# Optimization experiments

Hardware: AMD Instinct MI355X
Metric: run time of the kernel (lower is better)

## Reference

```python
import jax, jax.numpy as jnp
import numpy as np
from jax import lax

N, K, T_OBS, PRED = 64, 48, 30, 15
EMB, NODE, EDGE, ATT, CNN = 64, 128, 256, 64, 512


def setup_inputs():
    key = jax.random.key(0)
    ks = jax.random.split(key, 18)
    rn = lambda k, s, sc=1.0: jax.random.normal(k, s, jnp.float32) * sc
    return {
        "img_embedding": rn(ks[0], (N, CNN)),
        "target_obs_pos_abs": rn(ks[1], (N, T_OBS, 2)),
        "target_obs_pos_rel": rn(ks[2], (N, T_OBS, 2)),
        "target_obs_pos_step": rn(ks[3], (N, T_OBS, 2), 0.1),
        "nearby_obs_pos_abs": rn(ks[4], (N, K, T_OBS, 2)),
        "nearby_obs_pos_rel": rn(ks[5], (N, K, T_OBS, 2)),
        "nearby_obs_pos_step": rn(ks[6], (N, K, T_OBS, 2), 0.1),
        "target_obs_hist_size": jax.random.randint(ks[7], (N, 1), 0, T_OBS),
        "nearby_obs_hist_sizes": jax.random.randint(ks[8], (N, K, 1), 0, T_OBS),
        "W_disp": rn(ks[9], (EMB, 2), 0.1), "b_disp": jnp.zeros((EMB,), jnp.float32),
        "Wih_t": rn(ks[10], (4 * NODE, EMB), 0.05), "Whh_t": rn(ks[11], (4 * NODE, NODE), 0.05),
        "bih_t": jnp.zeros((4 * NODE,), jnp.float32), "bhh_t": jnp.zeros((4 * NODE,), jnp.float32),
        "Wih_n": rn(ks[12], (4 * EDGE, EMB), 0.05), "Whh_n": rn(ks[13], (4 * EDGE, EDGE), 0.05),
        "bih_n": jnp.zeros((4 * EDGE,), jnp.float32), "bhh_n": jnp.zeros((4 * EDGE,), jnp.float32),
        "W_att_t": rn(ks[14], (ATT, 2), 0.1), "b_att_t": jnp.zeros((ATT,), jnp.float32),
        "W_att_n": rn(ks[15], (ATT, 2), 0.1), "b_att_n": jnp.zeros((ATT,), jnp.float32),
        "W_pred": rn(ks[16], (2, NODE + CNN + EDGE), 0.02), "b_pred": jnp.zeros((2,), jnp.float32),
    }


def _lstm_cell(x, h, c, Wih, Whh, bih, bhh):
    # PyTorch LSTM gate order: i, f, g, o
    g = x @ Wih.T + h @ Whh.T + bih + bhh
    i, f, gg, o = jnp.split(g, 4, axis=-1)
    c2 = jax.nn.sigmoid(f) * c + jax.nn.sigmoid(i) * jnp.tanh(gg)
    return jax.nn.sigmoid(o) * jnp.tanh(c2), c2


def _forward(img_embedding, target_obs_pos_abs, target_obs_pos_rel, target_obs_pos_step,
             nearby_obs_pos_abs, nearby_obs_pos_rel, nearby_obs_pos_step,
             W_disp, b_disp, Wih_t, Whh_t, bih_t, bhh_t, Wih_n, Whh_n, bih_n, bhh_n,
             W_att_t, b_att_t, W_att_n, b_att_n, W_pred, b_pred,
             target_obs_hist_size, nearby_obs_hist_sizes):
    t_hist = target_obs_hist_size[:, 0]          # [N]
    n_hist = nearby_obs_hist_sizes[:, :, 0]      # [N, K]
    M = N * K

    def step(carry, t):
        tht, tct, nht, nct, Ht, cabs, crel, cstep, nabs, nstep = carry
        is_obs = t < T_OBS
        tc = jnp.minimum(t, T_OBS - 1)
        # prediction branch (only takes effect when t >= T_OBS)
        pred_out = jnp.concatenate([tht, img_embedding, Ht], 1) @ W_pred.T + b_pred  # [N,2]
        cabs = jnp.where(is_obs, target_obs_pos_abs[:, tc], cabs + pred_out)
        crel = jnp.where(is_obs, target_obs_pos_rel[:, tc], crel + pred_out)
        cstep = jnp.where(is_obs, target_obs_pos_step[:, tc], pred_out)
        nabs = jnp.where(is_obs, nearby_obs_pos_abs[:, :, tc], nabs)
        nstep = jnp.where(is_obs, nearby_obs_pos_step[:, :, tc], nstep)
        tmask = jnp.where(is_obs, t_hist > T_OBS - t, True)   # [N] bool
        nmask = jnp.where(is_obs, n_hist > T_OBS - t, True)   # [N,K] bool
        gate_t = jnp.sum(tmask) > 0  # emulates 'continue' when no target observed
        # target LSTM step, masked scatter-back
        th2, tc2 = _lstm_cell(cstep @ W_disp.T + b_disp, tht, tct, Wih_t, Whh_t, bih_t, bhh_t)
        u = (tmask & gate_t)[:, None]
        tht = jnp.where(u, th2, tht)
        tct = jnp.where(u, tc2, tct)
        # nearby LSTM step, masked scatter-back
        currN = jnp.sum(nmask)
        gate_n = gate_t & (currN > 0)
        nh2, nc2 = _lstm_cell(nstep.reshape(M, 2) @ W_disp.T + b_disp, nht, nct, Wih_n, Whh_n, bih_n, bhh_n)
        un = (nmask.reshape(M) & gate_n)[:, None]
        nht = jnp.where(un, nh2, nht)
        nct = jnp.where(un, nc2, nct)
        # social attention over padded nearby dim
        an = (nabs - cabs[:, None, :]) @ W_att_n.T + b_att_n   # [N,K,ATT]
        at = crel @ W_att_t.T + b_att_t                        # [N,ATT]
        mf = nmask.astype(jnp.float32)
        sc = jnp.einsum('nka,na->nk', an, at) * currN.astype(jnp.float32) / jnp.sqrt(jnp.float32(ATT))
        sc = sc * mf
        num = jnp.exp(sc - jnp.max(sc, 1, keepdims=True)) * mf
        w = num / (jnp.sum(num, 1, keepdims=True) + 1e-6)
        Ht = jnp.where(gate_n, jnp.einsum('nke,nk->ne', nht.reshape(N, K, EDGE), w), Ht)
        return (tht, tct, nht, nct, Ht, cabs, crel, cstep, nabs, nstep), crel

    z = lambda s: jnp.zeros(s, jnp.float32)
    init = (z((N, NODE)), z((N, NODE)), z((M, EDGE)), z((M, EDGE)), z((N, EDGE)),
            z((N, 2)), z((N, 2)), z((N, 2)), z((N, K, 2)), z((N, K, 2)))
    _, rels = lax.scan(step, init, jnp.arange(1, T_OBS + PRED))
    # last PRED emitted crel values are pred_traj[:, 0:PRED]
    return jnp.transpose(rels[-PRED:], (1, 0, 2))


def reference(img_embedding, target_obs_pos_abs, target_obs_pos_rel, target_obs_pos_step,
              nearby_obs_pos_abs, nearby_obs_pos_rel, nearby_obs_pos_step,
              target_obs_hist_size, nearby_obs_hist_sizes,
              W_disp, b_disp, Wih_t, Whh_t, bih_t, bhh_t, Wih_n, Whh_n, bih_n, bhh_n,
              W_att_t, b_att_t, W_att_n, b_att_n, W_pred, b_pred):
    return _forward(img_embedding, target_obs_pos_abs, target_obs_pos_rel, target_obs_pos_step,
                    nearby_obs_pos_abs, nearby_obs_pos_rel, nearby_obs_pos_step,
                    W_disp, b_disp, Wih_t, Whh_t, bih_t, bhh_t, Wih_n, Whh_n, bih_n, bhh_n,
                    W_att_t, b_att_t, W_att_n, b_att_n, W_pred, b_pred,
                    target_obs_hist_size, nearby_obs_hist_sizes)
```

## Files before the change

kernel.cpp:

```cpp
#include <hip/hip_runtime.h>
#include <math.h>

#define NT 64
#define KN 48
#define TOBS 30
#define NPRED 15
#define EMB 64
#define NODE 128
#define EDGE 256
#define ATTD 64
#define CNN 512
#define GNN 1024
#define GTT 512
#define TMAX 44

typedef _Float16 f16;
typedef f16 f16x8 __attribute__((ext_vector_type(8)));
typedef f16 f16x2 __attribute__((ext_vector_type(2)));
typedef float f32x4 __attribute__((ext_vector_type(4)));

__device__ __forceinline__ float rcp_f(float x) { return __builtin_amdgcn_rcpf(x); }
__device__ __forceinline__ float sigm(float x) { return rcp_f(1.f + __expf(-x)); }
__device__ __forceinline__ float tanh_f(float x) {
  float xx = fminf(fmaxf(x, -20.f), 20.f);
  float e = __expf(-2.f * xx);
  return (1.f - e) * rcp_f(1.f + e);
}
__device__ __forceinline__ unsigned ldcoh(const unsigned* p) {
  return __hip_atomic_load(p, __ATOMIC_RELAXED, __HIP_MEMORY_SCOPE_AGENT);
}
__device__ __forceinline__ float ldcohf(const float* p) {
  unsigned u = __hip_atomic_load((const unsigned*)p, __ATOMIC_RELAXED, __HIP_MEMORY_SCOPE_AGENT);
  return __builtin_bit_cast(float, u);
}
__device__ __forceinline__ void stcoh(unsigned* p, unsigned v) {
  __hip_atomic_store(p, v, __ATOMIC_RELAXED, __HIP_MEMORY_SCOPE_AGENT);
}
__device__ __forceinline__ void stcohf(float* p, float v) {
  __hip_atomic_store((unsigned*)p, __builtin_bit_cast(unsigned, v),
                     __ATOMIC_RELAXED, __HIP_MEMORY_SCOPE_AGENT);
}

__global__ __launch_bounds__(512) void prep_kernel(
    const float* __restrict__ Wih_n, const float* __restrict__ Whh_n,
    const float* __restrict__ bih_n, const float* __restrict__ bhh_n,
    const float* __restrict__ Wih_t, const float* __restrict__ Whh_t,
    const float* __restrict__ bih_t, const float* __restrict__ bhh_t,
    const float* __restrict__ W_disp, const float* __restrict__ b_disp,
    const int* __restrict__ t_hist, const int* __restrict__ n_hist,
    f16* __restrict__ Wn, f16* __restrict__ Wt, float* __restrict__ Ptv,
    float* __restrict__ bias_n, float* __restrict__ bias_t,
    int* __restrict__ gt_arr, int* __restrict__ gn_arr, float* __restrict__ cn_arr,
    int* __restrict__ last29p, unsigned* __restrict__ flags)
{
  const int gid = blockIdx.x * 512 + threadIdx.x;
  const int nthr = gridDim.x * 512;
  __shared__ int sgn[TMAX + 1];

  if (gid < 2 * NT) flags[gid] = 0u;

  for (int idx = gid; idx < GNN * 288; idx += nthr) {
    const int j    = idx & 7;
    const int lane = (idx >> 3) & 63;
    const int g    = (idx >> 9) & 3;
    const int r    = idx >> 11;
    const int u    = r % 9;
    const int s    = r / 9;
    const int w    = s & 7;
    const int h    = s >> 3;
    const int col = g * 256 + h * 128 + w * 16 + (lane & 15);
    float v = 0.f;
    if (u == 0) {
      if ((lane >> 4) == 0 && j < 3) {
        float acc = 0.f;
        for (int e = 0; e < EMB; ++e) {
          const float sel = (j == 0) ? W_disp[e * 2]
                          : (j == 1) ? W_disp[e * 2 + 1] : b_disp[e];
          acc += sel * Wih_n[col * EMB + e];
        }
        v = acc;
      }
    } else {
      const int k = (u - 1) * 32 + (lane >> 4) * 8 + j;
      v = Whh_n[col * EDGE + k];
    }
    Wn[idx] = (f16)v;
  }
  for (int idx = gid; idx < GTT * 192; idx += nthr) {
    const int j = idx & 7;
    const int col = (idx >> 3) & 511;
    const int c8 = idx >> 12;
    const int k = c8 * 8 + j;
    const float v = (k < EMB) ? Wih_t[col * EMB + k] : Whh_t[col * NODE + (k - EMB)];
    Wt[idx] = (f16)v;
  }
  for (int idx = gid; idx < 3 * GTT; idx += nthr) {
    const int sel = idx / GTT;
    const int col = idx - sel * GTT;
    float acc = 0.f;
    for (int e = 0; e < EMB; ++e) {
      const float sv = (sel == 0) ? W_disp[e * 2]
                     : (sel == 1) ? W_disp[e * 2 + 1] : b_disp[e];
      acc += sv * Wih_t[col * EMB + e];
    }
    Ptv[sel * GTT + col] = acc;
  }
  for (int idx = gid; idx < GNN; idx += nthr) bias_n[idx] = bih_n[idx] + bhh_n[idx];
  for (int idx = gid; idx < GTT; idx += nthr) bias_t[idx] = bih_t[idx] + bhh_t[idx];

  if (blockIdx.x == 0 && threadIdx.x < 352) {
    const int t = (threadIdx.x >> 3) + 1;
    const int part = threadIdx.x & 7;
    int any_t = 0, cnt = 0;
    if (t < TOBS) {
      const int thr = TOBS - t;
      for (int nn = part; nn < NT; nn += 8) any_t |= (t_hist[nn] > thr) ? 1 : 0;
      for (int m = part; m < NT * KN; m += 8) cnt += (n_hist[m] > thr) ? 1 : 0;
    } else { any_t = (part == 0); cnt = (part == 0) ? NT * KN : 0; }
    #pragma unroll
    for (int off = 1; off < 8; off <<= 1) {
      any_t |= __shfl_xor(any_t, off);
      cnt   += __shfl_xor(cnt, off);
    }
    if (part == 0) {
      const int gn = (any_t && cnt > 0) ? 1 : 0;
      gt_arr[t] = any_t;
      gn_arr[t] = gn;
      cn_arr[t] = (float)cnt;
      sgn[t] = gn;
    }
  }
  __syncthreads();
  if (blockIdx.x == 0 && threadIdx.x == 0) {
    int l = 30;
    for (int t = 29; t >= 1; --t) if (sgn[t]) { l = t; break; }
    last29p[0] = l;
  }
}

__global__ __launch_bounds__(512, 2) void model_kernel(
    const float* __restrict__ img, const float* __restrict__ tabs,
    const float* __restrict__ trel, const float* __restrict__ tstep,
    const float* __restrict__ nabs_g, const float* __restrict__ nstep_g,
    const int* __restrict__ thist_g, const int* __restrict__ nhist_g,
    const float* __restrict__ W_att_t, const float* __restrict__ b_att_t,
    const float* __restrict__ W_att_n, const float* __restrict__ b_att_n,
    const float* __restrict__ W_pred, const float* __restrict__ b_pred,
    const f16* __restrict__ Wn, const f16* __restrict__ Wt,
    const float* __restrict__ Ptv,
    const float* __restrict__ bias_n, const float* __restrict__ bias_t,
    const int* __restrict__ gt_arr, const int* __restrict__ gn_arr,
    const float* __restrict__ cn_arr, const int* __restrict__ last29p,
    unsigned* __restrict__ flags, unsigned* __restrict__ Hglob,
    float* __restrict__ Tglob,
    float* __restrict__ out)
{
  __shared__ f16 s_wlds[3 * 16384];
  __shared__ f16 s_virt[KN][32];
  __shared__ f16 Ah[KN][264];
  __shared__ float s_tht[NODE];
  __shared__ float s_tct[64];
  __shared__ f16  s_th16[NODE];
  __shared__ float s_Ht[EDGE];
  __shared__ float s_g[256];
  __shared__ float s_bt[256];
  __shared__ float s_sc[KN], s_w[KN];
  __shared__ float s_scal[8];
  __shared__ float s_dd[4];
  __shared__ float s_pimg[2];
  __shared__ int   s_nh[KN];
  __shared__ float s_wp[2][384];
  __shared__ float s_wan0[ATTD], s_wan1[ATTD], s_ban[ATTD];
  __shared__ float s_wat0[ATTD], s_wat1[ATTD], s_bat[ATTD];

  const int tid  = threadIdx.x;
  const int n    = blockIdx.x & 63;
  const int hb   = blockIdx.x >> 6;
  const int w    = tid >> 6;
  const int lane = tid & 63;
  const int cl   = lane & 15;
  const int kq   = lane >> 4;
  const int koff = kq * 8;

  for (int i = tid; i < KN * 264; i += 512) ((f16*)Ah)[i] = (f16)0.f;
  for (int i = tid; i < KN * 32; i += 512)
    s_virt[i >> 5][i & 31] = ((i & 31) == 2) ? (f16)1.f : (f16)0.f;
  for (int i = tid; i < NODE; i += 512) { s_tht[i] = 0.f; s_th16[i] = (f16)0.f; }
  if (tid < 64) s_tct[tid] = 0.f;
  for (int i = tid; i < EDGE; i += 512) s_Ht[i] = 0.f;
  if (tid < 256) {
    const int g = tid >> 6, dl = tid & 63;
    s_bt[tid] = bias_t[g * 128 + hb * 64 + dl];
  }
  for (int i = tid; i < 768; i += 512) {
    const int ww = i / 384, j = i - ww * 384;
    s_wp[ww][j] = (j < 128) ? W_pred[ww * 896 + j] : W_pred[ww * 896 + 640 + (j - 128)];
  }
  if (tid < KN) s_nh[tid] = nhist_g[n * KN + tid];
  if (tid < 8) s_scal[tid] = 0.f;
  if (tid >= 64 && tid < 128) {
    const int a = tid - 64;
    s_wan0[a] = W_att_n[a * 2]; s_wan1[a] = W_att_n[a * 2 + 1]; s_ban[a] = b_att_n[a];
  }
  if (tid >= 128 && tid < 192) {
    const int a = tid - 128;
    s_wat0[a] = W_att_t[a * 2]; s_wat1[a] = W_att_t[a * 2 + 1]; s_bat[a] = b_att_t[a];
  }
  const int thist = thist_g[n];
  const int last29 = last29p[0];

  float pt0 = 0.f, pt1 = 0.f, ptb = 0.f;
  if (tid < 256) {
    const int col = (tid >> 6) * 128 + hb * 64 + (tid & 63);
    pt0 = Ptv[col]; pt1 = Ptv[512 + col]; ptb = Ptv[1024 + col];
  }

  for (int i = tid; i < 3 * 8 * 256; i += 512) {
    const int c  = i & 255;
    const int wv = (i >> 8) & 7;
    const int u  = i >> 11;
    const size_t gbase = ((size_t)((hb * 8 + wv) * 9 + u)) * 2048;
    *(f16x8*)(s_wlds + (size_t)(u * 8 + wv) * 2048 + c * 8) =
        *(const f16x8*)(Wn + gbase + c * 8);
  }

  if (w < 2) {
    float s = 0.f;
    for (int j = lane; j < CNN; j += 64) s += img[n * CNN + j] * W_pred[w * 896 + 128 + j];
    for (int off = 32; off; off >>= 1) s += __shfl_down(s, off);
    if (lane == 0) s_pimg[w] = s + b_pred[w];
  }

  float creg[3][4];
  #pragma unroll
  for (int b = 0; b < 3; ++b)
    #pragma unroll
    for (int c = 0; c < 4; ++c) creg[b][c] = 0.f;

  float bias_q[4];
  #pragma unroll
  for (int g = 0; g < 4; ++g) bias_q[g] = bias_n[g * 256 + hb * 128 + w * 16 + cl];

  const f16* gW = Wn + ((size_t)(hb * 8 + w) * 9) * 2048 + (size_t)lane * 8;
  const f16* lW = s_wlds + (size_t)w * 2048 + (size_t)lane * 8;
  const int e_g = hb * 128 + w * 16 + cl;
  unsigned* myflag = flags + n * 2 + hb;
  unsigned* otflag = flags + n * 2 + (1 - hb);
  int bn = 0;

  __syncthreads();

  {
    if (tid < 96) {
      const int row = tid >> 1, comp = tid & 1;
      s_virt[row][comp] = (f16)nstep_g[((n * KN + row) * TOBS + 1) * 2 + comp];
    }
    if (tid < 2) {
      s_scal[tid]     = tabs[(n * TOBS + 1) * 2 + tid];
      s_scal[2 + tid] = trel[(n * TOBS + 1) * 2 + tid];
      s_scal[4 + tid] = tstep[(n * TOBS + 1) * 2 + tid];
    }
    if (tid >= 384 && tid < 448) {
      const int a = tid - 384;
      const float r0 = trel[(n * TOBS + 1) * 2 + 0], r1 = trel[(n * TOBS + 1) * 2 + 1];
      const float at = r0 * s_wat0[a] + r1 * s_wat1[a] + s_bat[a];
      float p0 = at * s_wan0[a], p1 = at * s_wan1[a], pb = at * s_ban[a];
      #pragma unroll
      for (int off = 32; off; off >>= 1) {
        p0 += __shfl_xor(p0, off); p1 += __shfl_xor(p1, off); pb += __shfl_xor(pb, off);
      }
      if (a == 0) { s_dd[0] = p0; s_dd[1] = p1; s_dd[2] = pb; }
    }
  }
  __syncthreads();

  for (int t = 1; t <= TMAX; ++t) {
    const bool is_obs = (t < TOBS);
    const int tc = is_obs ? t : (TOBS - 1);
    const int gate_t = gt_arr[t];
    const int gate_n = gn_arr[t];
    const float currN = cn_arr[t];
    const bool tmask = is_obs ? (thist > (TOBS - t)) : true;
    const bool do_t = gate_t && tmask;
    const bool need_x = (gate_n || do_t);
    const bool do_att = gate_n && (t >= last29);
    const int par = bn & 1;

    if (!is_obs) {
      if (w < 2) {
        float s = 0.f;
        for (int j = lane; j < NODE; j += 64) s += s_tht[j] * s_wp[w][j];
        for (int j = lane; j < EDGE; j += 64) s += s_Ht[j] * s_wp[w][128 + j];
        for (int off = 32; off; off >>= 1) s += __shfl_down(s, off);
        if (lane == 0) {
          const float p = s + s_pimg[w];
          const float cabs = s_scal[w] + p;
          const float crel = s_scal[2 + w] + p;
          s_scal[w] = cabs; s_scal[2 + w] = crel; s_scal[4 + w] = p;
          if (hb == 0) out[(n * NPRED + (t - TOBS)) * 2 + w] = crel;
        }
      }
      __syncthreads();
      if (tid >= 384 && tid < 448) {
        const int a = tid - 384;
        const float at = s_scal[2] * s_wat0[a] + s_scal[3] * s_wat1[a] + s_bat[a];
        float p0 = at * s_wan0[a], p1 = at * s_wan1[a], pb = at * s_ban[a];
        #pragma unroll
        for (int off = 32; off; off >>= 1) {
          p0 += __shfl_xor(p0, off); p1 += __shfl_xor(p1, off); pb += __shfl_xor(pb, off);
        }
        if (a == 0) { s_dd[0] = p0; s_dd[1] = p1; s_dd[2] = pb; }
      }
      __syncthreads();
    }

    f16 hreg[3][4];
    if (gate_n) {
      f32x4 acc[3][4];
      #pragma unroll
      for (int rt = 0; rt < 3; ++rt)
        #pragma unroll
        for (int g = 0; g < 4; ++g) acc[rt][g] = (f32x4){0.f, 0.f, 0.f, 0.f};

      #pragma unroll
      for (int u = 0; u < 9; ++u) {
        f16x8 bf[4];
        if (u < 3) {
          #pragma unroll
          for (int g = 0; g < 4; ++g)
            bf[g] = *(const f16x8*)(lW + u * 16384 + g * 512);
        } else {
          #pragma unroll
          for (int g = 0; g < 4; ++g)
            bf[g] = *(const f16x8*)(gW + u * 2048 + g * 512);
        }
        f16x8 af[3];
        #pragma unroll
        for (int rt = 0; rt < 3; ++rt) {
          const int row = rt * 16 + cl;
          const f16* ap = (u == 0) ? &s_virt[row][koff]
                                   : &Ah[row][(u - 1) * 32 + koff];
          af[rt] = *(const f16x8*)ap;
        }
        #pragma unroll
        for (int g = 0; g < 4; ++g)
          #pragma unroll
          for (int rt = 0; rt < 3; ++rt)
            acc[rt][g] = __builtin_amdgcn_mfma_f32_16x16x32_f16(af[rt], bf[g], acc[rt][g], 0, 0, 0);
      }

      unsigned* Hg = Hglob + (size_t)(par * NT + n) * (KN * 128);
      #pragma unroll
      for (int rt = 0; rt < 3; ++rt) {
        #pragma unroll
        for (int jj = 0; jj < 4; ++jj) {
          const int row = rt * 16 + kq * 4 + jj;
          const bool nm = is_obs ? (s_nh[row] > (TOBS - t)) : true;
          f16 hv;
          if (nm) {
            const float iv = acc[rt][0][jj] + bias_q[0];
            const float fv = acc[rt][1][jj] + bias_q[1];
            const float gv = acc[rt][2][jj] + bias_q[2];
            const float ov = acc[rt][3][jj] + bias_q[3];
            const float c2 = sigm(fv) * creg[rt][jj] + sigm(iv) * tanh_f(gv);
            creg[rt][jj] = c2;
            hv = (f16)(sigm(ov) * tanh_f(c2));
          } else {
            hv = Ah[row][e_g];
          }
          hreg[rt][jj] = hv;
          const unsigned lo = (unsigned)__builtin_bit_cast(unsigned short, hv);
          const unsigned hi = (unsigned)__shfl_down((int)lo, 1);
          if (!(cl & 1))
            stcoh(Hg + row * 128 + (e_g >> 1), lo | (hi << 16));
        }
      }
    }

    if (do_t && tid < 256) {
      float g0 = s_bt[tid] + s_scal[4] * pt0 + s_scal[5] * pt1 + ptb;
      float g1 = 0.f, g2 = 0.f, g3 = 0.f;
      const f16x2* th2 = (const f16x2*)s_th16;
      const f16x8* wp = (const f16x8*)(Wt + ((tid >> 6) * 128 + hb * 64 + (tid & 63)) * 8);
      #pragma unroll
      for (int c8 = 0; c8 < 16; ++c8) {
        const f16x8 wv = wp[(c8 + 8) * 512];
        f16x2 w0 = {wv[0], wv[1]}, w1 = {wv[2], wv[3]};
        f16x2 w2 = {wv[4], wv[5]}, w3 = {wv[6], wv[7]};
        g0 = __builtin_amdgcn_fdot2(w0, th2[c8 * 4 + 0], g0, false);
        g1 = __builtin_amdgcn_fdot2(w1, th2[c8 * 4 + 1], g1, false);
        g2 = __builtin_amdgcn_fdot2(w2, th2[c8 * 4 + 2], g2, false);
        g3 = __builtin_amdgcn_fdot2(w3, th2[c8 * 4 + 3], g3, false);
      }
      s_g[tid] = (g0 + g1) + (g2 + g3);
    }
    if (do_att && tid >= 256 && tid < 256 + KN) {
      const int k = tid - 256;
      const float a0 = nabs_g[((n * KN + k) * TOBS + tc) * 2 + 0] - s_scal[0];
      const float a1 = nabs_g[((n * KN + k) * TOBS + tc) * 2 + 1] - s_scal[1];
      const bool nm = is_obs ? (s_nh[k] > (TOBS - t)) : true;
      const float sc = (a0 * s_dd[0] + a1 * s_dd[1] + s_dd[2]) * currN * 0.125f;
      s_sc[k] = nm ? sc : 0.f;
      s_w[k]  = nm ? 1.f : 0.f;
    }
    __syncthreads();

    if (do_t && tid < 64) {
      const int d = hb * 64 + tid;
      const float iv = s_g[tid], fv = s_g[64 + tid];
      const float gv = s_g[128 + tid], ov = s_g[192 + tid];
      const float c2 = sigm(fv) * s_tct[tid] + sigm(iv) * tanh_f(gv);
      s_tct[tid] = c2;
      const float nh = sigm(ov) * tanh_f(c2);
      s_tht[d] = nh;
      s_th16[d] = (f16)nh;
      stcohf(Tglob + ((size_t)(par * NT + n) * 2 + hb) * 64 + tid, nh);
    }
    if (do_att && w == 4) {
      const bool act = lane < KN;
      const float sc = act ? s_sc[lane] : -1.0e30f;
      const float mf = act ? s_w[lane] : 0.f;
      float mx = sc;
      #pragma unroll
      for (int off = 32; off; off >>= 1) mx = fmaxf(mx, __shfl_xor(mx, off));
      float num = __expf(sc - mx) * mf;
      float sum = num;
      #pragma unroll
      for (int off = 32; off; off >>= 1) sum += __shfl_xor(sum, off);
      if (act) s_w[lane] = num * rcp_f(sum + 1e-6f);
    }
    __syncthreads();

    if (need_x && tid == 0) {
      stcoh(myflag, (unsigned)(bn + 1));
    }

    {
      const int tn = t + 1;
      if (tn <= TOBS) {
        const int tcn = (tn < TOBS) ? tn : (TOBS - 1);
        if (tid < 96) {
          const int row = tid >> 1, comp = tid & 1;
          s_virt[row][comp] = (f16)nstep_g[((n * KN + row) * TOBS + tcn) * 2 + comp];
        }
      }
      if (tn < TOBS) {
        if (tid < 2) {
          s_scal[tid]     = tabs[(n * TOBS + tn) * 2 + tid];
          s_scal[2 + tid] = trel[(n * TOBS + tn) * 2 + tid];
          s_scal[4 + tid] = tstep[(n * TOBS + tn) * 2 + tid];
        }
        if (tid >= 384 && tid < 448) {
          const int a = tid - 384;
          const float r0 = trel[(n * TOBS + tn) * 2 + 0], r1 = trel[(n * TOBS + tn) * 2 + 1];
          const float at = r0 * s_wat0[a] + r1 * s_wat1[a] + s_bat[a];
          float p0 = at * s_wan0[a], p1 = at * s_wan1[a], pb = at * s_ban[a];
          #pragma unroll
          for (int off = 32; off; off >>= 1) {
            p0 += __shfl_xor(p0, off); p1 += __shfl_xor(p1, off); pb += __shfl_xor(pb, off);
          }
          if (a == 0) { s_dd[0] = p0; s_dd[1] = p1; s_dd[2] = pb; }
        }
      }
    }

    if (need_x && tid == 0) {
      const unsigned step = (unsigned)(bn + 1);
      while (ldcoh(otflag) < step)
        __builtin_amdgcn_s_sleep(1);
    }
    __syncthreads();

    if (gate_n) {
      const unsigned* Hg = Hglob + (size_t)(par * NT + n) * (KN * 128);
      const int ob = (1 - hb) * 64;
      for (int i = tid; i < KN * 64; i += 512) {
        const int row = i >> 6, c = i & 63;
        const unsigned v = ldcoh(Hg + row * 128 + ob + c);
        *(unsigned*)&Ah[row][(ob + c) * 2] = v;
      }
      #pragma unroll
      for (int rt = 0; rt < 3; ++rt)
        #pragma unroll
        for (int jj = 0; jj < 4; ++jj)
          Ah[rt * 16 + kq * 4 + jj][e_g] = hreg[rt][jj];
    }
    if (do_t && tid >= 448) {
      const int dl = tid - 448;
      const int d = (1 - hb) * 64 + dl;
      const float nh = ldcohf(Tglob + ((size_t)(par * NT + n) * 2 + (1 - hb)) * 64 + dl);
      s_tht[d] = nh;
      s_th16[d] = (f16)nh;
    }
    __syncthreads();

    if (do_att && tid < EDGE) {
      float h0 = 0.f, h1 = 0.f, h2 = 0.f, h3 = 0.f;
      #pragma unroll
      for (int k = 0; k < KN; k += 4) {
        h0 += (float)Ah[k][tid]     * s_w[k];
        h1 += (float)Ah[k + 1][tid] * s_w[k + 1];
        h2 += (float)Ah[k + 2][tid] * s_w[k + 2];
        h3 += (float)Ah[k + 3][tid] * s_w[k + 3];
      }
      s_Ht[tid] = (h0 + h1) + (h2 + h3);
    }
    if (need_x) bn++;
    if (t >= 29) __syncthreads();
  }
}

extern "C" void kernel_launch(void* const* d_in, const int* in_sizes, int n_in,
                              void* d_out, int out_size, void* d_ws, size_t ws_size,
                              hipStream_t stream) {
  const float* img    = (const float*)d_in[0];
  const float* tabs   = (const float*)d_in[1];
  const float* trel   = (const float*)d_in[2];
  const float* tstep  = (const float*)d_in[3];
  const float* nabs   = (const float*)d_in[4];
  const float* nstep  = (const float*)d_in[6];
  const int*   thist  = (const int*)d_in[7];
  const int*   nhist  = (const int*)d_in[8];
  const float* W_disp = (const float*)d_in[9];
  const float* b_disp = (const float*)d_in[10];
  const float* Wih_t  = (const float*)d_in[11];
  const float* Whh_t  = (const float*)d_in[12];
  const float* bih_t  = (const float*)d_in[13];
  const float* bhh_t  = (const float*)d_in[14];
  const float* Wih_n  = (const float*)d_in[15];
  const float* Whh_n  = (const float*)d_in[16];
  const float* bih_n  = (const float*)d_in[17];
  const float* bhh_n  = (const float*)d_in[18];
  const float* W_att_t = (const float*)d_in[19];
  const float* b_att_t = (const float*)d_in[20];
  const float* W_att_n = (const float*)d_in[21];
  const float* b_att_n = (const float*)d_in[22];
  const float* W_pred  = (const float*)d_in[23];
  const float* b_pred  = (const float*)d_in[24];

  char* ws = (char*)d_ws;
  f16*      Wn      = (f16*)(ws);
  f16*      Wt      = (f16*)(ws + 655360);
  float*    bias_n  = (float*)(ws + 851968);
  float*    bias_t  = (float*)(ws + 856064);
  int*      gt_arr  = (int*)(ws + 858112);
  int*      gn_arr  = (int*)(ws + 858304);
  float*    cn_arr  = (float*)(ws + 858496);
  int*      last29p = (int*)(ws + 859648);
  unsigned* flags   = (unsigned*)(ws + 860160);
  float*    Ptv     = (float*)(ws + 901120);
  unsigned* Hglob   = (unsigned*)(ws + 1048576);
  float*    Tglob   = (float*)(ws + 4194304);

  prep_kernel<<<64, 512, 0, stream>>>(Wih_n, Whh_n, bih_n, bhh_n, Wih_t, Whh_t,
                                      bih_t, bhh_t, W_disp, b_disp,
                                      thist, nhist, Wn, Wt, Ptv,
                                      bias_n, bias_t, gt_arr, gn_arr, cn_arr,
                                      last29p, flags);
  model_kernel<<<2 * NT, 512, 0, stream>>>(img, tabs, trel, tstep, nabs, nstep,
                                           thist, nhist,
                                           W_att_t, b_att_t, W_att_n, b_att_n,
                                           W_pred, b_pred,
                                           Wn, Wt, Ptv, bias_n, bias_t,
                                           gt_arr, gn_arr, cn_arr, last29p,
                                           flags, Hglob, Tglob,
                                           (float*)d_out);
}
```

Measured before the change: 634.6 us.

## Read peer half of edge hidden state directly from global in MFMA loop

Stops staging the partner block's half of the edge-LSTM hidden state into LDS each step. The MFMA A-fragments and the attention-weighted sum now load that half straight from the coherent global buffer, and only the block's own half stays in a smaller LDS array. This removes a bulk copy pass from the per-step critical section and shrinks LDS use. In exchange the inner GEMM loop issues scalar coherent global loads, which have higher latency than LDS reads, and the global H buffer is now zeroed in the prep kernel.

```diff
diff --git a/kernel.cpp b/kernel.cpp
--- a/kernel.cpp
+++ b/kernel.cpp
@@ -40,6 +40,16 @@
   __hip_atomic_store((unsigned*)p, __builtin_bit_cast(unsigned, v),
                      __ATOMIC_RELAXED, __HIP_MEMORY_SCOPE_AGENT);
 }
+__device__ __forceinline__ f16x8 ld_hpair4(const unsigned* p) {
+  union { unsigned u4[4]; f16x8 v; } cv;
+  cv.u4[0] = ldcoh(p);     cv.u4[1] = ldcoh(p + 1);
+  cv.u4[2] = ldcoh(p + 2); cv.u4[3] = ldcoh(p + 3);
+  return cv.v;
+}
+__device__ __forceinline__ float f16half(unsigned wv, int hi) {
+  unsigned short s = (unsigned short)(hi ? (wv >> 16) : (wv & 0xffffu));
+  return (float)__builtin_bit_cast(f16, s);
+}
 
 __global__ __launch_bounds__(512) void prep_kernel(
     const float* __restrict__ Wih_n, const float* __restrict__ Whh_n,
@@ -51,13 +61,15 @@
     f16* __restrict__ Wn, f16* __restrict__ Wt, float* __restrict__ Ptv,
     float* __restrict__ bias_n, float* __restrict__ bias_t,
     int* __restrict__ gt_arr, int* __restrict__ gn_arr, float* __restrict__ cn_arr,
-    int* __restrict__ last29p, unsigned* __restrict__ flags)
+    int* __restrict__ last29p, unsigned* __restrict__ flags,
+    unsigned* __restrict__ Hglob)
 {
   const int gid = blockIdx.x * 512 + threadIdx.x;
   const int nthr = gridDim.x * 512;
   __shared__ int sgn[TMAX + 1];
 
   if (gid < 2 * NT) flags[gid] = 0u;
+  for (int idx = gid; idx < 2 * NT * KN * 128; idx += nthr) Hglob[idx] = 0u;
 
   for (int idx = gid; idx < GNN * 288; idx += nthr) {
     const int j    = idx & 7;
@@ -157,7 +169,7 @@
 {
   __shared__ f16 s_wlds[3 * 16384];
   __shared__ f16 s_virt[KN][32];
-  __shared__ f16 Ah[KN][264];
+  __shared__ f16 Ah[KN][136];
   __shared__ float s_tht[NODE];
   __shared__ float s_tct[64];
   __shared__ f16  s_th16[NODE];
@@ -182,7 +194,7 @@
   const int kq   = lane >> 4;
   const int koff = kq * 8;
 
-  for (int i = tid; i < KN * 264; i += 512) ((f16*)Ah)[i] = (f16)0.f;
+  for (int i = tid; i < KN * 136; i += 512) ((f16*)Ah)[i] = (f16)0.f;
   for (int i = tid; i < KN * 32; i += 512)
     s_virt[i >> 5][i & 31] = ((i & 31) == 2) ? (f16)1.f : (f16)0.f;
   for (int i = tid; i < NODE; i += 512) { s_tht[i] = 0.f; s_th16[i] = (f16)0.f; }
@@ -243,10 +255,12 @@
 
   const f16* gW = Wn + ((size_t)(hb * 8 + w) * 9) * 2048 + (size_t)lane * 8;
   const f16* lW = s_wlds + (size_t)w * 2048 + (size_t)lane * 8;
-  const int e_g = hb * 128 + w * 16 + cl;
+  const int own_u0 = 1 + hb * 4;
+  const int lcol = w * 16 + cl;
   unsigned* myflag = flags + n * 2 + hb;
   unsigned* otflag = flags + n * 2 + (1 - hb);
   int bn = 0;
+  int hbuf = 1;
 
   __syncthreads();
 
@@ -316,6 +330,7 @@
 
     f16 hreg[3][4];
     if (gate_n) {
+      const unsigned* Hgp = Hglob + (size_t)(hbuf * NT + n) * (KN * 128);
       f32x4 acc[3][4];
       #pragma unroll
       for (int rt = 0; rt < 3; ++rt)
@@ -338,9 +353,13 @@
         #pragma unroll
         for (int rt = 0; rt < 3; ++rt) {
           const int row = rt * 16 + cl;
-          const f16* ap = (u == 0) ? &s_virt[row][koff]
-                                   : &Ah[row][(u - 1) * 32 + koff];
-          af[rt] = *(const f16x8*)ap;
+          if (u == 0) {
+            af[rt] = *(const f16x8*)&s_virt[row][koff];
+          } else if (u >= own_u0 && u < own_u0 + 4) {
+            af[rt] = *(const f16x8*)&Ah[row][(u - own_u0) * 32 + koff];
+          } else {
+            af[rt] = ld_hpair4(Hgp + row * 128 + (u - 1) * 16 + kq * 4);
+          }
         }
         #pragma unroll
         for (int g = 0; g < 4; ++g)
@@ -366,13 +385,13 @@
             creg[rt][jj] = c2;
             hv = (f16)(sigm(ov) * tanh_f(c2));
           } else {
-            hv = Ah[row][e_g];
+            hv = Ah[row][lcol];
           }
           hreg[rt][jj] = hv;
           const unsigned lo = (unsigned)__builtin_bit_cast(unsigned short, hv);
           const unsigned hi = (unsigned)__shfl_down((int)lo, 1);
           if (!(cl & 1))
-            stcoh(Hg + row * 128 + (e_g >> 1), lo | (hi << 16));
+            stcoh(Hg + row * 128 + ((hb * 128 + lcol) >> 1), lo | (hi << 16));
         }
       }
     }
@@ -472,18 +491,12 @@
     __syncthreads();
 
     if (gate_n) {
-      const unsigned* Hg = Hglob + (size_t)(par * NT + n) * (KN * 128);
-      const int ob = (1 - hb) * 64;
-      for (int i = tid; i < KN * 64; i += 512) {
-        const int row = i >> 6, c = i & 63;
-        const unsigned v = ldcoh(Hg + row * 128 + ob + c);
-        *(unsigned*)&Ah[row][(ob + c) * 2] = v;
-      }
       #pragma unroll
       for (int rt = 0; rt < 3; ++rt)
         #pragma unroll
         for (int jj = 0; jj < 4; ++jj)
-          Ah[rt * 16 + kq * 4 + jj][e_g] = hreg[rt][jj];
+          Ah[rt * 16 + kq * 4 + jj][lcol] = hreg[rt][jj];
+      hbuf = par;
     }
     if (do_t && tid >= 448) {
       const int dl = tid - 448;
@@ -495,13 +508,27 @@
     __syncthreads();
 
     if (do_att && tid < EDGE) {
+      const bool ownh = ((tid >> 7) == hb);
+      const unsigned* Hgc = Hglob + (size_t)(par * NT + n) * (KN * 128) + (tid >> 1);
+      const int hi16 = tid & 1;
+      const int lc = tid & 127;
       float h0 = 0.f, h1 = 0.f, h2 = 0.f, h3 = 0.f;
-      #pragma unroll
-      for (int k = 0; k < KN; k += 4) {
-        h0 += (float)Ah[k][tid]     * s_w[k];
-        h1 += (float)Ah[k + 1][tid] * s_w[k + 1];
-        h2 += (float)Ah[k + 2][tid] * s_w[k + 2];
-        h3 += (float)Ah[k + 3][tid] * s_w[k + 3];
+      if (ownh) {
+        #pragma unroll
+        for (int k = 0; k < KN; k += 4) {
+          h0 += (float)Ah[k][lc]     * s_w[k];
+          h1 += (float)Ah[k + 1][lc] * s_w[k + 1];
+          h2 += (float)Ah[k + 2][lc] * s_w[k + 2];
+          h3 += (float)Ah[k + 3][lc] * s_w[k + 3];
+        }
+      } else {
+        #pragma unroll
+        for (int k = 0; k < KN; k += 4) {
+          h0 += f16half(ldcoh(Hgc + (k)     * 128), hi16) * s_w[k];
+          h1 += f16half(ldcoh(Hgc + (k + 1) * 128), hi16) * s_w[k + 1];
+          h2 += f16half(ldcoh(Hgc + (k + 2) * 128), hi16) * s_w[k + 2];
+          h3 += f16half(ldcoh(Hgc + (k + 3) * 128), hi16) * s_w[k + 3];
+        }
       }
       s_Ht[tid] = (h0 + h1) + (h2 + h3);
     }
@@ -556,7 +583,7 @@
                                       bih_t, bhh_t, W_disp, b_disp,
                                       thist, nhist, Wn, Wt, Ptv,
                                       bias_n, bias_t, gt_arr, gn_arr, cn_arr,
-                                      last29p, flags);
+                                      last29p, flags, Hglob);
   model_kernel<<<2 * NT, 512, 0, stream>>>(img, tabs, trel, tstep, nabs, nstep,
                                            thist, nhist,
                                            W_att_t, b_att_t, W_att_n, b_att_n,
```

Result: slower. 1.105 ms (+74.1%).
